# Kernel optimization log

Hardware: AMD Instinct MI355X
Metric: run time of the kernel (lower is better)

The kernel has to match this reference:

```python
import jax, jax.numpy as jnp
import numpy as np

TH = 1.0            # q_threshold for all IF neurons
POS_MAX = 7.0       # level//2 - 1, level=16, sym=True
NEG_MIN = -8.0      # -(level//2)
PREFIRE = 0.2       # attn_softmax_IF.prefire
S_QUANT = 7.0       # spiking_softmax scale = level//2 - 1
NUM_HEADS = 8


def if_step(x, vmem0, acc0, th=TH, pos_max=POS_MAX, neg_min=NEG_MIN):
    """One timestep of a symmetric ST-BIF neuron with straight-through surrogate.
    Forward: spike in {-1,0,+1}*th gated by membrane and accumulator saturation.
    Backward: identity (STE), accumulator is a constant."""
    acc0f = acc0.astype(x.dtype)
    v = vmem0 + x
    pos = jnp.logical_and(v >= th, acc0f < pos_max)
    neg = jnp.logical_and(v < 0.0, acc0f > neg_min)
    spike = pos.astype(x.dtype) - neg.astype(x.dtype)
    out_hard = spike * th
    out = x + jax.lax.stop_gradient(out_hard - x)  # STE: fwd=spike*th, bwd=identity
    acc = jax.lax.stop_gradient(acc0f + spike)     # running spike count (constant wrt grads)
    return out, acc


def setup_inputs() -> dict:
    key = jax.random.key(0)
    ks = jax.random.split(key, 16)
    B, N, C, H = 4, 1024, 512, NUM_HEADS
    D = C // H
    f32 = jnp.float32
    inp = {
        "x": jax.random.normal(ks[0], (B, N, C), dtype=f32),
        "w_qkv": jax.random.normal(ks[1], (3 * C, C), dtype=f32) * 0.02,
        "b_qkv": jnp.zeros((3 * C,), dtype=f32),
        "w_proj": jax.random.normal(ks[2], (C, C), dtype=f32) * 0.02,
        "b_proj": jnp.zeros((C,), dtype=f32),
        "q_vmem": jax.random.uniform(ks[3], (B, H, N, D), dtype=f32),
        "k_vmem": jax.random.uniform(ks[4], (B, H, N, D), dtype=f32),
        "v_vmem": jax.random.uniform(ks[5], (B, H, N, D), dtype=f32),
        "attn_vmem": jax.random.uniform(ks[6], (B, H, N, N), dtype=f32),
        "q_acc0": jax.random.randint(ks[7], (B, H, N, D), 0, 8).astype(jnp.int32),
        "k_acc0": jax.random.randint(ks[8], (B, H, N, D), 0, 8).astype(jnp.int32),
        "v_acc0": jax.random.randint(ks[9], (B, H, N, D), 0, 8).astype(jnp.int32),
        "attn_acc0": jax.random.randint(ks[10], (B, H, N, N), 0, 8).astype(jnp.int32),
    }
    return inp


def reference(x, w_qkv, b_qkv, w_proj, b_proj,
              q_vmem, k_vmem, v_vmem, attn_vmem,
              q_acc0, k_acc0, v_acc0, attn_acc0):
    B, N, C = x.shape
    H = NUM_HEADS
    D = C // H
    scale = D ** -0.5
    sg = jax.lax.stop_gradient

    # qkv projection -> [3, B, H, N, D]
    qkv = (x @ w_qkv.T + b_qkv).reshape(B, N, 3, H, D).transpose(2, 0, 3, 1, 4)
    q_in, k_in, v_in = qkv[0], qkv[1], qkv[2]

    # ST-BIF IF neurons (one timestep, carried state)
    q_s, q_acc = if_step(q_in, q_vmem, q_acc0)
    k_s, k_acc = if_step(k_in, k_vmem, k_acc0)
    v_s, v_acc = if_step(v_in, v_vmem, v_acc0)

    q = q_s * scale
    # accumulator corrections: acc_q * q_threshold (*scale for q) minus detached spike output
    q_corr = sg(q_acc * TH * scale - q)
    k_corr = sg(k_acc * TH - k_s)
    v_corr = sg(v_acc * TH - v_s)

    # multi: (q + q_corr) @ k^T + q @ k_corr^T   -> [B, H, N, N]
    attn = (jnp.einsum('bhnd,bhmd->bhnm', q + q_corr, k_s)
            + jnp.einsum('bhnd,bhmd->bhnm', q, k_corr))

    # spiking softmax substitute: softmax of the (accumulated) scores, scaled to quant range
    attn = jax.nn.softmax(attn, axis=-1) * S_QUANT

    # attn_softmax_IF with prefire bias on the membrane
    attn_s, attn_acc = if_step(attn, attn_vmem + PREFIRE * TH, attn_acc0)
    attn_corr = sg(attn_acc * TH - attn_s)

    # multi1: (attn + attn_corr) @ v + attn @ v_corr  -> [B, H, N, D]
    out = (jnp.einsum('bhnm,bhmd->bhnd', attn_s + attn_corr, v_s)
           + jnp.einsum('bhnm,bhmd->bhnd', attn_s, v_corr))

    # after_attn_IF: fresh state (rounding init 0.5*th, zero accumulator)
    out, _ = if_step(out, jnp.asarray(0.5 * TH, out.dtype), jnp.zeros_like(out))

    out = out.transpose(0, 2, 1, 3).reshape(B, N, C)
    return out @ w_proj.T + b_proj
```

## Files before the change

### kernel.cpp

```cpp
#include <hip/hip_runtime.h>
#include <hip/hip_bf16.h>
#include <cstdint>

typedef short short8 __attribute__((ext_vector_type(8)));
typedef float f32x4 __attribute__((ext_vector_type(4)));
typedef int   int4v __attribute__((ext_vector_type(4)));
typedef _Float16 fp16x8 __attribute__((ext_vector_type(8)));

using bf16 = __hip_bfloat16;

#define MFMA16(a, b, c) __builtin_amdgcn_mfma_f32_16x16x32_bf16((a), (b), (c), 0, 0, 0)
#define MFMAI8(a, b, c) __builtin_amdgcn_mfma_i32_16x16x64_i8((a), (b), (c), 0, 0, 0)
#define MFMAF16(a, b, c) __builtin_amdgcn_mfma_f32_16x16x32_f16((a), (b), (c), 0, 0, 0)

__device__ __forceinline__ short8 ldb8(const bf16* p) {
    return *reinterpret_cast<const short8*>(p);
}
__device__ __forceinline__ int lo16(unsigned u) { return (int)(u << 16) >> 16; }
__device__ __forceinline__ int hi16(unsigned u) { return (int)u >> 16; }

__global__ __launch_bounds__(256) void k_prep(
    const float* __restrict__ X, const float* __restrict__ W, const float* __restrict__ Wp,
    _Float16* __restrict__ Xh, _Float16* __restrict__ Xl,
    _Float16* __restrict__ Wh, _Float16* __restrict__ Wl, bf16* __restrict__ Wpb)
{
    const int NX = 4096 * 512, NW = 1536 * 512, NP = 512 * 512;
    for (int i = blockIdx.x * 256 + threadIdx.x; i < NX + NW + NP; i += gridDim.x * 256) {
        if (i < NX) {
            const float v = X[i] * 512.0f;
            const _Float16 h = (_Float16)v;
            Xh[i] = h;
            Xl[i] = (_Float16)((v - (float)h) * 2048.0f);
        } else if (i < NX + NW) {
            const int j = i - NX;
            const float v = W[j] * 512.0f;
            const _Float16 h = (_Float16)v;
            Wh[j] = h;
            Wl[j] = (_Float16)((v - (float)h) * 2048.0f);
        } else {
            const int j = i - NX - NW;
            Wpb[j] = __float2bfloat16(Wp[j]);
        }
    }
}

__global__ __launch_bounds__(256, 3) void k_qkv_f16(
    const _Float16* __restrict__ Xh, const _Float16* __restrict__ Xl,
    const _Float16* __restrict__ Wh, const _Float16* __restrict__ Wl,
    const float* __restrict__ bq,
    const float* __restrict__ qvm, const float* __restrict__ kvm, const float* __restrict__ vvm,
    const int* __restrict__ qac, const int* __restrict__ kac, const int* __restrict__ vac,
    int8_t* __restrict__ Q2, int8_t* __restrict__ K2c,
    int8_t* __restrict__ VsT, int8_t* __restrict__ VaT)
{
    __shared__ alignas(16) _Float16 XhL[64 * 32];
    __shared__ alignas(16) _Float16 XlL[64 * 32];
    __shared__ alignas(16) _Float16 WhL[128 * 32];
    __shared__ alignas(16) _Float16 WlL[128 * 32];

    const int tid = threadIdx.x;
    const int w = tid >> 6, lane = tid & 63, lo = lane & 15, hi = lane >> 4;
    const int wr = w >> 1, wc = w & 1;
    const int r0w = blockIdx.y * 64 + wr * 32;
    const int c0w = blockIdx.x * 128 + wc * 64;

    const int srow = tid >> 2, sk8 = tid & 3;
    const _Float16* gxh  = Xh + (size_t)(blockIdx.y * 64 + srow) * 512 + sk8 * 8;
    const _Float16* gxl  = Xl + (size_t)(blockIdx.y * 64 + srow) * 512 + sk8 * 8;
    const _Float16* gw0h = Wh + (size_t)(blockIdx.x * 128 + srow) * 512 + sk8 * 8;
    const _Float16* gw1h = Wh + (size_t)(blockIdx.x * 128 + 64 + srow) * 512 + sk8 * 8;
    const _Float16* gw0l = Wl + (size_t)(blockIdx.x * 128 + srow) * 512 + sk8 * 8;
    const _Float16* gw1l = Wl + (size_t)(blockIdx.x * 128 + 64 + srow) * 512 + sk8 * 8;

    float4 sxh, sxl, sw0h, sw1h, sw0l, sw1l;
#define QISSUE(kc) { const int off_ = (kc) * 32; \
    sxh  = *reinterpret_cast<const float4*>(gxh  + off_); \
    sxl  = *reinterpret_cast<const float4*>(gxl  + off_); \
    sw0h = *reinterpret_cast<const float4*>(gw0h + off_); \
    sw1h = *reinterpret_cast<const float4*>(gw1h + off_); \
    sw0l = *reinterpret_cast<const float4*>(gw0l + off_); \
    sw1l = *reinterpret_cast<const float4*>(gw1l + off_); }

    QISSUE(0)

    f32x4 hh[2][4] = {};
    f32x4 md[2][4] = {};

    for (int kc = 0; kc < 16; ++kc) {
        __syncthreads();
        *reinterpret_cast<float4*>(XhL + tid * 8)         = sxh;
        *reinterpret_cast<float4*>(XlL + tid * 8)         = sxl;
        *reinterpret_cast<float4*>(WhL + tid * 8)         = sw0h;
        *reinterpret_cast<float4*>(WhL + (tid + 256) * 8) = sw1h;
        *reinterpret_cast<float4*>(WlL + tid * 8)         = sw0l;
        *reinterpret_cast<float4*>(WlL + (tid + 256) * 8) = sw1l;
        if (kc < 15) QISSUE(kc + 1);
        __syncthreads();

        const fp16x8 Ah0 = *reinterpret_cast<const fp16x8*>(XhL + (wr * 32 + lo) * 32 + hi * 8);
        const fp16x8 Ah1 = *reinterpret_cast<const fp16x8*>(XhL + (wr * 32 + 16 + lo) * 32 + hi * 8);
        const fp16x8 Al0 = *reinterpret_cast<const fp16x8*>(XlL + (wr * 32 + lo) * 32 + hi * 8);
        const fp16x8 Al1 = *reinterpret_cast<const fp16x8*>(XlL + (wr * 32 + 16 + lo) * 32 + hi * 8);
        fp16x8 Bh[4], Bl[4];
        #pragma unroll
        for (int j = 0; j < 4; ++j) {
            const int cl = (wc * 64 + j * 16 + lo) * 32 + hi * 8;
            Bh[j] = *reinterpret_cast<const fp16x8*>(WhL + cl);
            Bl[j] = *reinterpret_cast<const fp16x8*>(WlL + cl);
        }
        #pragma unroll
        for (int j = 0; j < 4; ++j) {
            hh[0][j] = MFMAF16(Ah0, Bh[j], hh[0][j]);
            hh[1][j] = MFMAF16(Ah1, Bh[j], hh[1][j]);
            md[0][j] = MFMAF16(Ah0, Bl[j], md[0][j]);
            md[0][j] = MFMAF16(Al0, Bh[j], md[0][j]);
            md[1][j] = MFMAF16(Ah1, Bl[j], md[1][j]);
            md[1][j] = MFMAF16(Al1, Bh[j], md[1][j]);
        }
    }
#undef QISSUE

    const int sel = (unsigned)c0w >> 9;
    const float* VM = (sel == 0) ? qvm : (sel == 1) ? kvm : vvm;
    const int*   AC = (sel == 0) ? qac : (sel == 1) ? kac : vac;

    #pragma unroll
    for (int i = 0; i < 2; ++i) {
        const int rowb = r0w + i * 16 + hi * 4;
        const int b = rowb >> 10, nb = rowb & 1023;
        #pragma unroll
        for (int j = 0; j < 4; ++j) {
            const int c = c0w + j * 16 + lo;
            const int ch = c & 511;
            const int hh_ = ch >> 6, d = ch & 63;
            const int bh = b * 8 + hh_;
            const float bcol = bq[c];
            int sp[4], a4[4];
            #pragma unroll
            for (int r = 0; r < 4; ++r) {
                const size_t gi = (size_t)(bh * 1024 + nb + r) * 64 + d;
                const float vm = VM[gi];
                const int a0 = AC[gi];
                const float val = fmaf(md[i][j][r], 0x1p-11f, hh[i][j][r]) * 0x1p-18f;
                const float v_ = vm + (val + bcol);
                int s = ((v_ >= 1.0f) && (a0 < 7)) ? 1 : 0;
                if (v_ < 0.0f) s -= 1;
                sp[r] = s; a4[r] = a0;
            }
            if (sel == 2) {
                uchar4 us, ua;
                us.x = (uint8_t)sp[0]; us.y = (uint8_t)sp[1]; us.z = (uint8_t)sp[2]; us.w = (uint8_t)sp[3];
                ua.x = (uint8_t)(a4[0] + sp[0]); ua.y = (uint8_t)(a4[1] + sp[1]);
                ua.z = (uint8_t)(a4[2] + sp[2]); ua.w = (uint8_t)(a4[3] + sp[3]);
                const size_t vi = (size_t)(bh * 64 + d) * 1024 + nb;
                *reinterpret_cast<uchar4*>(VsT + vi) = us;
                *reinterpret_cast<uchar4*>(VaT + vi) = ua;
            } else {
                int8_t* base = ((sel == 0) ? Q2 : K2c) + (size_t)(bh * 1024 + nb) * 128 + d;
                #pragma unroll
                for (int r = 0; r < 4; ++r) {
                    const int v0 = (sel == 0) ? a4[r] + sp[r] : sp[r];
                    const int v1 = (sel == 0) ? sp[r]         : a4[r];
                    base[r * 128]      = (int8_t)v0;
                    base[r * 128 + 64] = (int8_t)v1;
                }
            }
        }
    }
}

__global__ __launch_bounds__(256, 4) void k_av0(
    const int* __restrict__ aac, const int8_t* __restrict__ VsT,
    uint8_t* __restrict__ aac8, int* __restrict__ AV0)
{
    const int w = threadIdx.x >> 6, lane = threadIdx.x & 63;
    const int lo = lane & 15, hi = lane >> 4;
    const int bh = blockIdx.y;
    const int hk = blockIdx.z;
    const int ko0 = hk * 512;
    const int row = blockIdx.x * 64 + w * 16 + lo;
    const size_t arow = ((size_t)bh * 1024 + row) * 1024;

    int4 buf[2][4];
    {
        const int4* ap0 = reinterpret_cast<const int4*>(aac + arow + ko0 + hi * 16);
        const int4* ap1 = reinterpret_cast<const int4*>(aac + arow + ko0 + 64 + hi * 16);
        #pragma unroll
        for (int j = 0; j < 4; ++j) { buf[0][j] = ap0[j]; buf[1][j] = ap1[j]; }
    }

    int4v acc[4] = {{0,0,0,0},{0,0,0,0},{0,0,0,0},{0,0,0,0}};
    #pragma unroll
    for (int tt = 0; tt < 8; ++tt) {
        int4 c[4];
        #pragma unroll
        for (int j = 0; j < 4; ++j) c[j] = buf[tt & 1][j];
        if (tt < 6) {
            const int4* ap = reinterpret_cast<const int4*>(aac + arow + ko0 + (tt + 2) * 64 + hi * 16);
            #pragma unroll
            for (int j = 0; j < 4; ++j) buf[tt & 1][j] = ap[j];
        }
        int4v af;
        af[0] = (int)(unsigned)(c[0].x | (c[0].y << 8) | (c[0].z << 16) | (c[0].w << 24));
        af[1] = (int)(unsigned)(c[1].x | (c[1].y << 8) | (c[1].z << 16) | (c[1].w << 24));
        af[2] = (int)(unsigned)(c[2].x | (c[2].y << 8) | (c[2].z << 16) | (c[2].w << 24));
        af[3] = (int)(unsigned)(c[3].x | (c[3].y << 8) | (c[3].z << 16) | (c[3].w << 24));
        *reinterpret_cast<int4v*>(aac8 + arow + ko0 + tt * 64 + hi * 16) = af;
        #pragma unroll
        for (int dt = 0; dt < 4; ++dt) {
            const int4v bf = *reinterpret_cast<const int4v*>(
                VsT + ((size_t)(bh * 64 + dt * 16 + lo)) * 1024 + ko0 + tt * 64 + hi * 16);
            acc[dt] = MFMAI8(af, bf, acc[dt]);
        }
    }
    int* outp = AV0 + (size_t)hk * 32 * 1024 * 64;
    #pragma unroll
    for (int dt = 0; dt < 4; ++dt)
        #pragma unroll
        for (int r = 0; r < 4; ++r)
            outp[((size_t)bh * 1024 + blockIdx.x * 64 + w * 16 + hi * 4 + r) * 64 + dt * 16 + lo] = acc[dt][r];
}

__global__ __launch_bounds__(256, 4) void k_attn(
    const int8_t* __restrict__ Q2, const int8_t* __restrict__ K2c,
    const float* __restrict__ avm, const uint8_t* __restrict__ aac8,
    const int8_t* __restrict__ Vsum, const int* __restrict__ AV0,
    bf16* __restrict__ O2)
{
    __shared__ alignas(16) char Sc[16896];
    int*   const maxb = (int*)(Sc + 16384);
    float* const sumb = (float*)(Sc + 16640);
    const int w = threadIdx.x >> 6, lane = threadIdx.x & 63;
    const int lo = lane & 15, hi = lane >> 4;
    const int bh = blockIdx.z * 8 + blockIdx.y;
    const int n0 = blockIdx.x * 16;

    unsigned pA[16][2];
    {
        const int8_t* qb = Q2 + ((size_t)(bh * 1024 + n0 + lo)) * 128 + hi * 16;
        const int4v qa0 = *reinterpret_cast<const int4v*>(qb);
        const int4v qa1 = *reinterpret_cast<const int4v*>(qb + 64);
        const int8_t* kbp = K2c + ((size_t)(bh * 1024 + w * 256 + lo)) * 128 + hi * 16;
        int4v b0[2], b1[2];
        b0[0] = *reinterpret_cast<const int4v*>(kbp);
        b1[0] = *reinterpret_cast<const int4v*>(kbp + 64);
        b0[1] = *reinterpret_cast<const int4v*>(kbp + 2048);
        b1[1] = *reinterpret_cast<const int4v*>(kbp + 2048 + 64);
        #pragma unroll
        for (int t = 0; t < 16; ++t) {
            const int4v c0f = b0[t & 1], c1f = b1[t & 1];
            if (t < 14) {
                const int8_t* np = kbp + (t + 2) * 2048;
                b0[t & 1] = *reinterpret_cast<const int4v*>(np);
                b1[t & 1] = *reinterpret_cast<const int4v*>(np + 64);
            }
            int4v s = {0, 0, 0, 0};
            s = MFMAI8(c0f, qa0, s);
            s = MFMAI8(c1f, qa1, s);
            pA[t][0] = (s[0] & 0xFFFF) | ((unsigned)s[1] << 16);
            pA[t][1] = (s[2] & 0xFFFF) | ((unsigned)s[3] << 16);
        }
    }

    const float*   vmp = avm  + ((size_t)(bh * 1024 + n0 + lo)) * 1024 + w * 256 + hi * 4;
    const uint8_t* acp = aac8 + ((size_t)(bh * 1024 + n0 + lo)) * 1024 + w * 256 + hi * 4;
    float4 vmr[4]; uchar4 acr[4];
#define PF(u) { vmr[(u)&3] = *reinterpret_cast<const float4*>(vmp + (u)*16); \
                acr[(u)&3] = *reinterpret_cast<const uchar4*>(acp + (u)*16); }
    PF(0) PF(1) PF(2) PF(3)

    int mxi = -32768;
    #pragma unroll
    for (int t = 0; t < 16; ++t) {
        mxi = max(mxi, max(max(lo16(pA[t][0]), hi16(pA[t][0])),
                           max(lo16(pA[t][1]), hi16(pA[t][1]))));
    }
    mxi = max(mxi, __shfl_xor(mxi, 16));
    mxi = max(mxi, __shfl_xor(mxi, 32));
    if (lane < 16) maxb[w * 16 + lo] = mxi;
    __syncthreads();
    const int M = max(max(maxb[lo], maxb[16 + lo]), max(maxb[32 + lo], maxb[48 + lo]));

    const float kls = 0.18033688011112042f;
    float sum = 0.f;
    #pragma unroll
    for (int t = 0; t < 16; ++t) {
        sum += exp2f(kls * (float)(lo16(pA[t][0]) - M));
        sum += exp2f(kls * (float)(hi16(pA[t][0]) - M));
        sum += exp2f(kls * (float)(lo16(pA[t][1]) - M));
        sum += exp2f(kls * (float)(hi16(pA[t][1]) - M));
    }
    sum += __shfl_xor(sum, 16);
    sum += __shfl_xor(sum, 32);
    if (lane < 16) sumb[w * 16 + lo] = sum;
    __syncthreads();
    const float rsum = 7.0f / ((sumb[lo] + sumb[16 + lo]) + (sumb[32 + lo] + sumb[48 + lo]));

    #pragma unroll
    for (int u = 0; u < 16; ++u) {
        const float4 vm = vmr[u & 3];
        const uchar4 a8 = acr[u & 3];
        if (u < 12) PF(u + 4)
        const int sv[4] = { lo16(pA[u][0]), hi16(pA[u][0]), lo16(pA[u][1]), hi16(pA[u][1]) };
        const float vr[4] = { vm.x, vm.y, vm.z, vm.w };
        const int   ar[4] = { a8.x, a8.y, a8.z, a8.w };
        unsigned pk = 0;
        #pragma unroll
        for (int i = 0; i < 4; ++i) {
            const float e_ = exp2f(kls * (float)(sv[i] - M));
            const float p7 = e_ * rsum;
            const float v_ = (vr[i] + 0.2f) + p7;
            const unsigned sp = ((v_ >= 1.0f) && (ar[i] < 7)) ? 1u : 0u;
            pk |= sp << (8 * i);
        }
        char* pb = Sc + lo * 1024 + ((w * 256 + u * 16 + hi * 4) ^ ((lo & 7) << 4));
        *reinterpret_cast<unsigned*>(pb) = pk;
    }
#undef PF
    __syncthreads();

    {
        const int d0 = w * 16;
        const int* avp = AV0 + ((size_t)(bh * 1024 + n0 + hi * 4)) * 64 + d0 + lo;
        int av[4];
        #pragma unroll
        for (int r = 0; r < 4; ++r)
            av[r] = avp[(size_t)r * 64] + avp[(size_t)r * 64 + (size_t)32 * 1024 * 64];

        const int8_t* vp = Vsum + ((size_t)(bh * 64 + d0 + lo)) * 1024 + hi * 16;
        int4v nv0 = *reinterpret_cast<const int4v*>(vp);
        int4v nv1 = *reinterpret_cast<const int4v*>(vp + 64);
        int4v acc = {0, 0, 0, 0};
        #pragma unroll
        for (int tt = 0; tt < 16; ++tt) {
            const int4v cv = (tt & 1) ? nv1 : nv0;
            if (tt < 14) {
                if (tt & 1) nv1 = *reinterpret_cast<const int4v*>(vp + (tt + 2) * 64);
                else        nv0 = *reinterpret_cast<const int4v*>(vp + (tt + 2) * 64);
            }
            const int ko = tt * 64 + hi * 16;
            const int4v a1 = *reinterpret_cast<const int4v*>(Sc + lo * 1024 + (ko ^ ((lo & 7) << 4)));
            acc = MFMAI8(a1, cv, acc);
        }
        #pragma unroll
        for (int r = 0; r < 4; ++r) {
            const int o = acc[r] + av[r];
            const float f = (float)o;
            const float o2 = (f >= 0.5f ? 1.f : 0.f) - (f < -0.5f ? 1.f : 0.f);
            const int n = n0 + hi * 4 + r;
            O2[((size_t)(blockIdx.z * 1024 + n)) * 512 + blockIdx.y * 64 + d0 + lo] = __float2bfloat16(o2);
        }
    }
}

__global__ __launch_bounds__(256) void k_proj(
    const bf16* __restrict__ O2, const bf16* __restrict__ W, const float* __restrict__ bias,
    float* __restrict__ Y)
{
    const int w = threadIdx.x >> 6, lane = threadIdx.x & 63;
    const int lo = lane & 15, hi = lane >> 4;
    const int r0 = blockIdx.y * 16;
    const int c0 = blockIdx.x * 256 + w * 64;

    f32x4 acc[4] = {{0.f,0.f,0.f,0.f},{0.f,0.f,0.f,0.f},{0.f,0.f,0.f,0.f},{0.f,0.f,0.f,0.f}};
    const bf16* op  = O2 + (size_t)(r0 + lo) * 512 + hi * 8;
    const bf16* wp0 = W + (size_t)(c0 + lo) * 512 + hi * 8;

    short8 a2[2], b2[2][4];
    a2[0] = ldb8(op);
    #pragma unroll
    for (int t = 0; t < 4; ++t) b2[0][t] = ldb8(wp0 + t * 16 * 512);

    #pragma unroll
    for (int kb = 0; kb < 16; ++kb) {
        const int cur = kb & 1, nxt = cur ^ 1;
        if (kb < 15) {
            a2[nxt] = ldb8(op + (kb + 1) * 32);
            #pragma unroll
            for (int t = 0; t < 4; ++t)
                b2[nxt][t] = ldb8(wp0 + t * 16 * 512 + (kb + 1) * 32);
        }
        #pragma unroll
        for (int t = 0; t < 4; ++t)
            acc[t] = MFMA16(a2[cur], b2[cur][t], acc[t]);
    }
    #pragma unroll
    for (int t = 0; t < 4; ++t) {
        const int col = c0 + t * 16 + lo;
        const float bcol = bias[col];
        #pragma unroll
        for (int r = 0; r < 4; ++r) {
            const int rr = r0 + hi * 4 + r;
            Y[(size_t)rr * 512 + col] = acc[t][r] + bcol;
        }
    }
}

extern "C" void kernel_launch(void* const* d_in, const int* in_sizes, int n_in,
                              void* d_out, int out_size, void* d_ws, size_t ws_size,
                              hipStream_t stream)
{
    const float* x     = (const float*)d_in[0];
    const float* wqkv  = (const float*)d_in[1];
    const float* bqkv  = (const float*)d_in[2];
    const float* wproj = (const float*)d_in[3];
    const float* bproj = (const float*)d_in[4];
    const float* qvm   = (const float*)d_in[5];
    const float* kvm   = (const float*)d_in[6];
    const float* vvm   = (const float*)d_in[7];
    const float* avm   = (const float*)d_in[8];
    const int*   qac   = (const int*)d_in[9];
    const int*   kac   = (const int*)d_in[10];
    const int*   vac   = (const int*)d_in[11];
    const int*   aac   = (const int*)d_in[12];

    char* p = (char*)d_ws;
    int8_t*   Q2   = (int8_t*)p;   p += (size_t)32 * 1024 * 128;
    int8_t*   K2c  = (int8_t*)p;   p += (size_t)32 * 1024 * 128;
    int8_t*   VsT  = (int8_t*)p;   p += (size_t)32 * 64 * 1024;
    int8_t*   VaT  = (int8_t*)p;   p += (size_t)32 * 64 * 1024;
    bf16*     O2   = (bf16*)p;     p += (size_t)4096 * 512 * 2;
    bf16*     Wpb  = (bf16*)p;     p += (size_t)512 * 512 * 2;
    _Float16* Xh   = (_Float16*)p; p += (size_t)4096 * 512 * 2;
    _Float16* Xl   = (_Float16*)p; p += (size_t)4096 * 512 * 2;
    _Float16* Wh   = (_Float16*)p; p += (size_t)1536 * 512 * 2;
    _Float16* Wl   = (_Float16*)p; p += (size_t)1536 * 512 * 2;
    uint8_t*  aac8 = (uint8_t*)p;  p += (size_t)32 * 1024 * 1024;
    int*      AV0  = (int*)p;      p += (size_t)2 * 32 * 1024 * 64 * 4;

    k_prep<<<dim3(2048), 256, 0, stream>>>(x, wqkv, wproj, Xh, Xl, Wh, Wl, Wpb);
    k_qkv_f16<<<dim3(12, 64), 256, 0, stream>>>(Xh, Xl, Wh, Wl, bqkv, qvm, kvm, vvm,
                                                qac, kac, vac, Q2, K2c, VsT, VaT);
    k_av0<<<dim3(16, 32, 2), 256, 0, stream>>>(aac, VsT, aac8, AV0);
    k_attn<<<dim3(64, 8, 4), 256, 0, stream>>>(Q2, K2c, avm, aac8, VaT, AV0, O2);
    k_proj<<<dim3(2, 256), 256, 0, stream>>>(O2, Wpb, bproj, (float*)d_out);
}
```

Measured before the change: 456.0 us.

## Fuse attn-acc times V product into attention kernel, drop k_av0 pass

Removes the separate k_av0 kernel that computed the attn_acc0 @ V_s partial product. The int32-to-int8 packing of attn_acc0 moves into the prep kernel, and the attention kernel now issues a second int8 MFMA per tile using the packed accumulator and V_s. This drops the AV0 intermediate write and read-back plus one launch, at the cost of doubling MFMA and load work inside k_attn. The projection kernel is also retiled to 32 columns per wave with twice as many blocks.

```diff
diff --git a/kernel.cpp b/kernel.cpp
--- a/kernel.cpp
+++ b/kernel.cpp
@@ -21,8 +21,10 @@
 
 __global__ __launch_bounds__(256) void k_prep(
     const float* __restrict__ X, const float* __restrict__ W, const float* __restrict__ Wp,
+    const int* __restrict__ aac,
     _Float16* __restrict__ Xh, _Float16* __restrict__ Xl,
-    _Float16* __restrict__ Wh, _Float16* __restrict__ Wl, bf16* __restrict__ Wpb)
+    _Float16* __restrict__ Wh, _Float16* __restrict__ Wl, bf16* __restrict__ Wpb,
+    uint8_t* __restrict__ aac8)
 {
     const int NX = 4096 * 512, NW = 1536 * 512, NP = 512 * 512;
     for (int i = blockIdx.x * 256 + threadIdx.x; i < NX + NW + NP; i += gridDim.x * 256) {
@@ -41,6 +43,12 @@
             const int j = i - NX - NW;
             Wpb[j] = __float2bfloat16(Wp[j]);
         }
+    }
+    const int NAG = 8388608;
+    for (int g = blockIdx.x * 256 + threadIdx.x; g < NAG; g += gridDim.x * 256) {
+        const int4 v = reinterpret_cast<const int4*>(aac)[g];
+        reinterpret_cast<unsigned*>(aac8)[g] =
+            (unsigned)(v.x | (v.y << 8) | (v.z << 16) | (v.w << 24));
     }
 }
 
@@ -169,62 +177,10 @@
     }
 }
 
-__global__ __launch_bounds__(256, 4) void k_av0(
-    const int* __restrict__ aac, const int8_t* __restrict__ VsT,
-    uint8_t* __restrict__ aac8, int* __restrict__ AV0)
-{
-    const int w = threadIdx.x >> 6, lane = threadIdx.x & 63;
-    const int lo = lane & 15, hi = lane >> 4;
-    const int bh = blockIdx.y;
-    const int hk = blockIdx.z;
-    const int ko0 = hk * 512;
-    const int row = blockIdx.x * 64 + w * 16 + lo;
-    const size_t arow = ((size_t)bh * 1024 + row) * 1024;
-
-    int4 buf[2][4];
-    {
-        const int4* ap0 = reinterpret_cast<const int4*>(aac + arow + ko0 + hi * 16);
-        const int4* ap1 = reinterpret_cast<const int4*>(aac + arow + ko0 + 64 + hi * 16);
-        #pragma unroll
-        for (int j = 0; j < 4; ++j) { buf[0][j] = ap0[j]; buf[1][j] = ap1[j]; }
-    }
-
-    int4v acc[4] = {{0,0,0,0},{0,0,0,0},{0,0,0,0},{0,0,0,0}};
-    #pragma unroll
-    for (int tt = 0; tt < 8; ++tt) {
-        int4 c[4];
-        #pragma unroll
-        for (int j = 0; j < 4; ++j) c[j] = buf[tt & 1][j];
-        if (tt < 6) {
-            const int4* ap = reinterpret_cast<const int4*>(aac + arow + ko0 + (tt + 2) * 64 + hi * 16);
-            #pragma unroll
-            for (int j = 0; j < 4; ++j) buf[tt & 1][j] = ap[j];
-        }
-        int4v af;
-        af[0] = (int)(unsigned)(c[0].x | (c[0].y << 8) | (c[0].z << 16) | (c[0].w << 24));
-        af[1] = (int)(unsigned)(c[1].x | (c[1].y << 8) | (c[1].z << 16) | (c[1].w << 24));
-        af[2] = (int)(unsigned)(c[2].x | (c[2].y << 8) | (c[2].z << 16) | (c[2].w << 24));
-        af[3] = (int)(unsigned)(c[3].x | (c[3].y << 8) | (c[3].z << 16) | (c[3].w << 24));
-        *reinterpret_cast<int4v*>(aac8 + arow + ko0 + tt * 64 + hi * 16) = af;
-        #pragma unroll
-        for (int dt = 0; dt < 4; ++dt) {
-            const int4v bf = *reinterpret_cast<const int4v*>(
-                VsT + ((size_t)(bh * 64 + dt * 16 + lo)) * 1024 + ko0 + tt * 64 + hi * 16);
-            acc[dt] = MFMAI8(af, bf, acc[dt]);
-        }
-    }
-    int* outp = AV0 + (size_t)hk * 32 * 1024 * 64;
-    #pragma unroll
-    for (int dt = 0; dt < 4; ++dt)
-        #pragma unroll
-        for (int r = 0; r < 4; ++r)
-            outp[((size_t)bh * 1024 + blockIdx.x * 64 + w * 16 + hi * 4 + r) * 64 + dt * 16 + lo] = acc[dt][r];
-}
-
 __global__ __launch_bounds__(256, 4) void k_attn(
     const int8_t* __restrict__ Q2, const int8_t* __restrict__ K2c,
     const float* __restrict__ avm, const uint8_t* __restrict__ aac8,
-    const int8_t* __restrict__ Vsum, const int* __restrict__ AV0,
+    const int8_t* __restrict__ Vsum, const int8_t* __restrict__ Vs,
     bf16* __restrict__ O2)
 {
     __shared__ alignas(16) char Sc[16896];
@@ -321,30 +277,42 @@
 
     {
         const int d0 = w * 16;
-        const int* avp = AV0 + ((size_t)(bh * 1024 + n0 + hi * 4)) * 64 + d0 + lo;
-        int av[4];
-        #pragma unroll
-        for (int r = 0; r < 4; ++r)
-            av[r] = avp[(size_t)r * 64] + avp[(size_t)r * 64 + (size_t)32 * 1024 * 64];
-
-        const int8_t* vp = Vsum + ((size_t)(bh * 64 + d0 + lo)) * 1024 + hi * 16;
-        int4v nv0 = *reinterpret_cast<const int4v*>(vp);
-        int4v nv1 = *reinterpret_cast<const int4v*>(vp + 64);
+        const int8_t*  sup = Vsum + ((size_t)(bh * 64 + d0 + lo)) * 1024 + hi * 16;
+        const int8_t*  vsp = Vs   + ((size_t)(bh * 64 + d0 + lo)) * 1024 + hi * 16;
+        const uint8_t* ap8 = aac8 + ((size_t)(bh * 1024 + n0 + lo)) * 1024 + hi * 16;
+
+        int4v nsu0 = *reinterpret_cast<const int4v*>(sup);
+        int4v nsu1 = *reinterpret_cast<const int4v*>(sup + 64);
+        int4v nvs0 = *reinterpret_cast<const int4v*>(vsp);
+        int4v nvs1 = *reinterpret_cast<const int4v*>(vsp + 64);
+        int4v nac0 = *reinterpret_cast<const int4v*>(ap8);
+        int4v nac1 = *reinterpret_cast<const int4v*>(ap8 + 64);
         int4v acc = {0, 0, 0, 0};
         #pragma unroll
         for (int tt = 0; tt < 16; ++tt) {
-            const int4v cv = (tt & 1) ? nv1 : nv0;
+            const int4v csu = (tt & 1) ? nsu1 : nsu0;
+            const int4v cvs = (tt & 1) ? nvs1 : nvs0;
+            const int4v cac = (tt & 1) ? nac1 : nac0;
             if (tt < 14) {
-                if (tt & 1) nv1 = *reinterpret_cast<const int4v*>(vp + (tt + 2) * 64);
-                else        nv0 = *reinterpret_cast<const int4v*>(vp + (tt + 2) * 64);
+                const int nb = (tt + 2) * 64;
+                if (tt & 1) {
+                    nsu1 = *reinterpret_cast<const int4v*>(sup + nb);
+                    nvs1 = *reinterpret_cast<const int4v*>(vsp + nb);
+                    nac1 = *reinterpret_cast<const int4v*>(ap8 + nb);
+                } else {
+                    nsu0 = *reinterpret_cast<const int4v*>(sup + nb);
+                    nvs0 = *reinterpret_cast<const int4v*>(vsp + nb);
+                    nac0 = *reinterpret_cast<const int4v*>(ap8 + nb);
+                }
             }
             const int ko = tt * 64 + hi * 16;
             const int4v a1 = *reinterpret_cast<const int4v*>(Sc + lo * 1024 + (ko ^ ((lo & 7) << 4)));
-            acc = MFMAI8(a1, cv, acc);
+            acc = MFMAI8(a1, csu, acc);
+            acc = MFMAI8(cac, cvs, acc);
         }
         #pragma unroll
         for (int r = 0; r < 4; ++r) {
-            const int o = acc[r] + av[r];
+            const int o = acc[r];
             const float f = (float)o;
             const float o2 = (f >= 0.5f ? 1.f : 0.f) - (f < -0.5f ? 1.f : 0.f);
             const int n = n0 + hi * 4 + r;
@@ -360,32 +328,31 @@
     const int w = threadIdx.x >> 6, lane = threadIdx.x & 63;
     const int lo = lane & 15, hi = lane >> 4;
     const int r0 = blockIdx.y * 16;
-    const int c0 = blockIdx.x * 256 + w * 64;
-
-    f32x4 acc[4] = {{0.f,0.f,0.f,0.f},{0.f,0.f,0.f,0.f},{0.f,0.f,0.f,0.f},{0.f,0.f,0.f,0.f}};
+    const int c0 = blockIdx.x * 128 + w * 32;
+
+    f32x4 acc[2] = {{0.f,0.f,0.f,0.f},{0.f,0.f,0.f,0.f}};
     const bf16* op  = O2 + (size_t)(r0 + lo) * 512 + hi * 8;
     const bf16* wp0 = W + (size_t)(c0 + lo) * 512 + hi * 8;
-
-    short8 a2[2], b2[2][4];
+    const bf16* wp1 = W + (size_t)(c0 + 16 + lo) * 512 + hi * 8;
+
+    short8 a2[2], b2[2][2];
     a2[0] = ldb8(op);
-    #pragma unroll
-    for (int t = 0; t < 4; ++t) b2[0][t] = ldb8(wp0 + t * 16 * 512);
+    b2[0][0] = ldb8(wp0);
+    b2[0][1] = ldb8(wp1);
 
     #pragma unroll
     for (int kb = 0; kb < 16; ++kb) {
         const int cur = kb & 1, nxt = cur ^ 1;
         if (kb < 15) {
-            a2[nxt] = ldb8(op + (kb + 1) * 32);
-            #pragma unroll
-            for (int t = 0; t < 4; ++t)
-                b2[nxt][t] = ldb8(wp0 + t * 16 * 512 + (kb + 1) * 32);
-        }
-        #pragma unroll
-        for (int t = 0; t < 4; ++t)
-            acc[t] = MFMA16(a2[cur], b2[cur][t], acc[t]);
-    }
-    #pragma unroll
-    for (int t = 0; t < 4; ++t) {
+            a2[nxt]    = ldb8(op  + (kb + 1) * 32);
+            b2[nxt][0] = ldb8(wp0 + (kb + 1) * 32);
+            b2[nxt][1] = ldb8(wp1 + (kb + 1) * 32);
+        }
+        acc[0] = MFMA16(a2[cur], b2[cur][0], acc[0]);
+        acc[1] = MFMA16(a2[cur], b2[cur][1], acc[1]);
+    }
+    #pragma unroll
+    for (int t = 0; t < 2; ++t) {
         const int col = c0 + t * 16 + lo;
         const float bcol = bias[col];
         #pragma unroll
@@ -426,12 +393,10 @@
     _Float16* Wh   = (_Float16*)p; p += (size_t)1536 * 512 * 2;
     _Float16* Wl   = (_Float16*)p; p += (size_t)1536 * 512 * 2;
     uint8_t*  aac8 = (uint8_t*)p;  p += (size_t)32 * 1024 * 1024;
-    int*      AV0  = (int*)p;      p += (size_t)2 * 32 * 1024 * 64 * 4;
-
-    k_prep<<<dim3(2048), 256, 0, stream>>>(x, wqkv, wproj, Xh, Xl, Wh, Wl, Wpb);
+
+    k_prep<<<dim3(2048), 256, 0, stream>>>(x, wqkv, wproj, aac, Xh, Xl, Wh, Wl, Wpb, aac8);
     k_qkv_f16<<<dim3(12, 64), 256, 0, stream>>>(Xh, Xl, Wh, Wl, bqkv, qvm, kvm, vvm,
                                                 qac, kac, vac, Q2, K2c, VsT, VaT);
-    k_av0<<<dim3(16, 32, 2), 256, 0, stream>>>(aac, VsT, aac8, AV0);
-    k_attn<<<dim3(64, 8, 4), 256, 0, stream>>>(Q2, K2c, avm, aac8, VaT, AV0, O2);
-    k_proj<<<dim3(2, 256), 256, 0, stream>>>(O2, Wpb, bproj, (float*)d_out);
-}
+    k_attn<<<dim3(64, 8, 4), 256, 0, stream>>>(Q2, K2c, avm, aac8, VaT, VsT, O2);
+    k_proj<<<dim3(4, 256), 256, 0, stream>>>(O2, Wpb, bproj, (float*)d_out);
+}
```

New measurement: 465.6 us. +2.1%, slower.
